# Optimization experiments

Measured on AMD Instinct MI355X. Metric: run time of the kernel, lower is better.

The kernel has to match this reference:

```python
import jax, jax.numpy as jnp
import numpy as np

N, E, F_IN, DIM, HEADS = 16384, 262144, 128, 64, 4
HID = DIM * HEADS  # 256
NEG = 0.2


def _lin(k, fan_in, fan_out):
    kw, kb = jax.random.split(k)
    s = 1.0 / np.sqrt(fan_in)
    return (jax.random.uniform(kw, (fan_in, fan_out), jnp.float32, -s, s),
            jax.random.uniform(kb, (fan_out,), jnp.float32, -s, s))


def setup_inputs() -> dict:
    key = jax.random.key(0)
    ks = jax.random.split(key, 20)
    x = jax.random.normal(ks[0], (N, F_IN), jnp.float32)
    edge_index = jax.random.randint(ks[1], (2, E), 0, N, jnp.int32)
    Win, b_in = _lin(ks[2], F_IN, DIM)
    Wskip, bskip = _lin(ks[3], DIM, HID)
    # conv1: in=DIM, out per head=DIM, heads=HEADS, concat -> HID
    Wl1, _ = _lin(ks[4], DIM, HID)
    Wr1, _ = _lin(ks[5], DIM, HID)
    att1 = jax.random.normal(ks[6], (HEADS, DIM), jnp.float32) * 0.1
    b1 = jnp.zeros((HID,), jnp.float32)
    # conv2: in=HID, out=HID, heads=1, concat=False
    Wl2, _ = _lin(ks[7], HID, HID)
    Wr2, _ = _lin(ks[8], HID, HID)
    att2 = jax.random.normal(ks[9], (1, HID), jnp.float32) * 0.1
    b2 = jnp.zeros((HID,), jnp.float32)
    # conv3: in=HID, out=HID, heads=1, concat=False
    Wl3, _ = _lin(ks[10], HID, HID)
    Wr3, _ = _lin(ks[11], HID, HID)
    att3 = jax.random.normal(ks[12], (1, HID), jnp.float32) * 0.1
    b3 = jnp.zeros((HID,), jnp.float32)
    Wm1, bm1 = _lin(ks[13], HID, DIM)
    Wm2, bm2 = _lin(ks[14], DIM, DIM)
    Wm3, bm3 = _lin(ks[15], DIM, 1)
    return dict(x=x, edge_index=edge_index, Win=Win, b_in=b_in,
                Wskip=Wskip, bskip=bskip,
                Wl1=Wl1, Wr1=Wr1, att1=att1, b1=b1,
                Wl2=Wl2, Wr2=Wr2, att2=att2, b2=b2,
                Wl3=Wl3, Wr3=Wr3, att3=att3, b3=b3,
                Wm1=Wm1, bm1=bm1, Wm2=Wm2, bm2=bm2, Wm3=Wm3, bm3=bm3)


def gatv2(x, src, dst, Wl, Wr, att, b, concat):
    # PyG GATv2Conv: x_l = lin_l(x)[src], x_r = lin_r(x)[dst]
    n = x.shape[0]
    H, D = att.shape
    xl = (x @ Wl).reshape(n, H, D)
    xr = (x @ Wr).reshape(n, H, D)
    e = jax.nn.leaky_relu(xl[src] + xr[dst], NEG)          # [E, H, D]
    logits = jnp.einsum('ehd,hd->eh', e, att)              # [E, H]
    m = jax.ops.segment_max(logits, dst, num_segments=n)   # per-dst softmax
    alpha = jnp.exp(logits - m[dst])
    denom = jax.ops.segment_sum(alpha, dst, num_segments=n)
    alpha = alpha / denom[dst]
    out = jax.ops.segment_sum(alpha[:, :, None] * xl[src], dst, num_segments=n)
    out = out.reshape(n, H * D) if concat else out.mean(axis=1)
    return out + b


def reference(x, edge_index, Win, b_in, Wskip, bskip,
              Wl1, Wr1, att1, b1, Wl2, Wr2, att2, b2,
              Wl3, Wr3, att3, b3, Wm1, bm1, Wm2, bm2, Wm3, bm3):
    n = x.shape[0]
    # add self loops (GATv2Conv default add_self_loops=True)
    loop = jnp.arange(n, dtype=edge_index.dtype)
    src = jnp.concatenate([edge_index[0], loop])
    dst = jnp.concatenate([edge_index[1], loop])

    h = jax.nn.relu(x @ Win + b_in)                         # [N, DIM]
    out1 = jax.nn.relu(gatv2(h, src, dst, Wl1, Wr1, att1, b1, True))
    out1 = out1 + (h @ Wskip + bskip)                       # [N, HID]
    out2 = jax.nn.relu(gatv2(out1, src, dst, Wl2, Wr2, att2, b2, False))
    out2 = out2 + out1
    out3 = jax.nn.relu(gatv2(out2, src, dst, Wl3, Wr3, att3, b3, False))
    out3 = out3 + out2
    out = jax.nn.relu(out3 @ Wm1 + bm1)
    out = jax.nn.relu(out @ Wm2 + bm2)
    out = out @ Wm3 + bm3                                   # [N, 1]
    return out.reshape(-1)
```

## Files before the change

### kernel.cpp

```cpp
#include <hip/hip_runtime.h>
#include <cstdint>
#include <cstddef>

#define N_NODES 16384
#define E_EDGES 262144
#define FIN     128
#define DIM     64
#define HID     256
#define NEG     0.2f

typedef _Float16 h8 __attribute__((ext_vector_type(8)));
typedef _Float16 h4 __attribute__((ext_vector_type(4)));
typedef float    f32x4 __attribute__((ext_vector_type(4)));

__global__ __launch_bounds__(256) void zero_cnt_kernel(int4* __restrict__ cnt) {
    cnt[blockIdx.x * 256 + threadIdx.x] = make_int4(0, 0, 0, 0);
}

__global__ __launch_bounds__(256) void hist_kernel(const int* __restrict__ dst,
                                                   int* __restrict__ cnt) {
    int i = blockIdx.x * 256 + threadIdx.x;
    if (i < E_EDGES) atomicAdd(&cnt[dst[i]], 1);
}

__global__ __launch_bounds__(256) void csr_scan_kernel(const int* __restrict__ cnt,
                                                       int* __restrict__ offs,
                                                       int* __restrict__ cursor) {
    __shared__ int bs[256];
    __shared__ int psum[257];
    int tid = threadIdx.x;
    int base = tid * 64;
    int s = 0;
    for (int i = 0; i < 64; ++i) s += cnt[base + i];
    bs[tid] = s;
    __syncthreads();
    if (tid == 0) {
        int r = 0;
        for (int i = 0; i < 256; ++i) { psum[i] = r; r += bs[i]; }
        psum[256] = r;
    }
    __syncthreads();
    int run = psum[tid];
    for (int i = 0; i < 64; ++i) {
        int c = cnt[base + i];
        offs[base + i] = run;
        cursor[base + i] = run;
        run += c;
    }
    if (tid == 255) offs[N_NODES] = run;
}

__global__ __launch_bounds__(256) void scatter_kernel(const int* __restrict__ src,
                                                      const int* __restrict__ dst,
                                                      int* __restrict__ cursor,
                                                      int* __restrict__ esrc) {
    int i = blockIdx.x * 256 + threadIdx.x;
    if (i < E_EDGES) {
        int p = atomicAdd(&cursor[dst[i]], 1);
        esrc[p] = src[i];
    }
}

struct PackJob { const float* W; _Float16* dst; int Ksrc, Nsrc, NT, colOff; };
struct PackJobs { PackJob j[9]; };

__global__ __launch_bounds__(256) void pack_all_kernel(PackJobs jobs) {
    PackJob jb = jobs.j[blockIdx.y];
    int i = blockIdx.x * 256 + threadIdx.x;
    if (i < jb.Ksrc * jb.Nsrc) {
        int k = i / jb.Nsrc, n = i % jb.Nsrc;
        jb.dst[((size_t)(k >> 3) * jb.NT + jb.colOff + n) * 8 + (k & 7)] = (_Float16)jb.W[i];
    }
}

__global__ __launch_bounds__(256) void cast16_kernel(const float* __restrict__ x,
                                                     _Float16* __restrict__ x16) {
    int i = blockIdx.x * 256 + threadIdx.x;
    float4 v = ((const float4*)x)[i];
    h4 o; o[0] = (_Float16)v.x; o[1] = (_Float16)v.y;
    o[2] = (_Float16)v.z; o[3] = (_Float16)v.w;
    ((h4*)x16)[i] = o;
}

template<int K, bool RELU, bool O16>
__global__ __launch_bounds__(256) void mfma_nt64_kernel(const _Float16* __restrict__ A,
                                                        const _Float16* __restrict__ Wp,
                                                        const float* __restrict__ bias,
                                                        void* __restrict__ outv) {
    int tid = threadIdx.x;
    int lane = tid & 63, wid = tid >> 6;
    int rowBase = blockIdx.x * 256 + wid * 64;
    int l15 = lane & 15, l4 = lane >> 4;

    f32x4 acc[4][4] = {};
#pragma unroll
    for (int ks = 0; ks < K / 32; ++ks) {
        h8 af[4], bf[4];
#pragma unroll
        for (int mi = 0; mi < 4; ++mi)
            af[mi] = *(const h8*)(A + (size_t)(rowBase + mi * 16 + l15) * K + ks * 32 + l4 * 8);
#pragma unroll
        for (int ni = 0; ni < 4; ++ni)
            bf[ni] = *(const h8*)(Wp + ((size_t)(ks * 4 + l4) * 64 + ni * 16 + l15) * 8);
#pragma unroll
        for (int mi = 0; mi < 4; ++mi)
#pragma unroll
            for (int ni = 0; ni < 4; ++ni)
                acc[mi][ni] = __builtin_amdgcn_mfma_f32_16x16x32_f16(af[mi], bf[ni], acc[mi][ni], 0, 0, 0);
    }
#pragma unroll
    for (int mi = 0; mi < 4; ++mi)
#pragma unroll
        for (int ni = 0; ni < 4; ++ni) {
            int c = ni * 16 + l15;
            float bv = bias[c];
#pragma unroll
            for (int q = 0; q < 4; ++q) {
                int r = rowBase + mi * 16 + l4 * 4 + q;
                float v = acc[mi][ni][q] + bv;
                if (RELU) v = fmaxf(v, 0.f);
                if constexpr (O16) ((_Float16*)outv)[(size_t)r * 64 + c] = (_Float16)v;
                else               ((float*)outv)[(size_t)r * 64 + c] = v;
            }
        }
}

template<int K>
__global__ __launch_bounds__(256) void mfma_gemm_kernel(const _Float16* __restrict__ A,
                                                        const _Float16* __restrict__ Wp,
                                                        int NT,
                                                        _Float16* __restrict__ o16a,
                                                        _Float16* __restrict__ o16b,
                                                        float* __restrict__ o32,
                                                        const float* __restrict__ bias) {
    int tid = threadIdx.x;
    int lane = tid & 63, wid = tid >> 6;
    int wm = wid >> 1, wn = wid & 1;
    int rowBase = blockIdx.x * 128 + wm * 64;
    int colBase = blockIdx.y * 128 + wn * 64;
    int l15 = lane & 15, l4 = lane >> 4;

    f32x4 acc[4][4] = {};
#pragma unroll
    for (int ks = 0; ks < K / 32; ++ks) {
        h8 af[4], bf[4];
#pragma unroll
        for (int mi = 0; mi < 4; ++mi)
            af[mi] = *(const h8*)(A + (size_t)(rowBase + mi * 16 + l15) * K + ks * 32 + l4 * 8);
#pragma unroll
        for (int ni = 0; ni < 4; ++ni)
            bf[ni] = *(const h8*)(Wp + ((size_t)(ks * 4 + l4) * NT + colBase + ni * 16 + l15) * 8);
#pragma unroll
        for (int mi = 0; mi < 4; ++mi)
#pragma unroll
            for (int ni = 0; ni < 4; ++ni)
                acc[mi][ni] = __builtin_amdgcn_mfma_f32_16x16x32_f16(af[mi], bf[ni], acc[mi][ni], 0, 0, 0);
    }

    int seg = colBase >> 8;
    int cbase = colBase & 255;
    if (o32 != nullptr && seg == 2) {
#pragma unroll
        for (int mi = 0; mi < 4; ++mi)
#pragma unroll
            for (int ni = 0; ni < 4; ++ni) {
                int c = cbase + ni * 16 + l15;
                float bv = bias[c];
#pragma unroll
                for (int q = 0; q < 4; ++q) {
                    int r = rowBase + mi * 16 + l4 * 4 + q;
                    o32[(size_t)r * 256 + c] = acc[mi][ni][q] + bv;
                }
            }
    } else {
        _Float16* o = (seg == 0) ? o16a : o16b;
#pragma unroll
        for (int mi = 0; mi < 4; ++mi)
#pragma unroll
            for (int ni = 0; ni < 4; ++ni) {
                int c = cbase + ni * 16 + l15;
#pragma unroll
                for (int q = 0; q < 4; ++q) {
                    int r = rowBase + mi * 16 + l4 * 4 + q;
                    o[(size_t)r * 256 + c] = (_Float16)acc[mi][ni][q];
                }
            }
    }
}

template<int H, int OMODE>
__global__ __launch_bounds__(256) void gat_agg_kernel(const _Float16* __restrict__ xl,
                                                      const _Float16* __restrict__ xr,
                                                      const float* __restrict__ att,
                                                      const float* __restrict__ bias,
                                                      const float* __restrict__ resid,
                                                      const int* __restrict__ offs,
                                                      const int* __restrict__ esrc,
                                                      float* __restrict__ out,
                                                      _Float16* __restrict__ out16) {
    int wid = threadIdx.x >> 6;
    int lane = threadIdx.x & 63;
    int node = blockIdx.x * 4 + wid;

    auto ld4 = [&](const _Float16* p, int n) -> float4 {
        h4 v = *(const h4*)(p + ((size_t)n << 8) + (lane << 2));
        return make_float4((float)v[0], (float)v[1], (float)v[2], (float)v[3]);
    };

    float4 xrv = ld4(xr, node);
    float4 av = ((const float4*)att)[lane];

    float m = -1e30f, s = 0.f;
    float4 acc = make_float4(0.f, 0.f, 0.f, 0.f);

    auto logit = [&](const float4& xlv) -> float {
        float ex = xlv.x + xrv.x; ex = ex > 0.f ? ex : NEG * ex;
        float ey = xlv.y + xrv.y; ey = ey > 0.f ? ey : NEG * ey;
        float ez = xlv.z + xrv.z; ez = ez > 0.f ? ez : NEG * ez;
        float ew = xlv.w + xrv.w; ew = ew > 0.f ? ew : NEG * ew;
        float lp = ex * av.x + ey * av.y + ez * av.z + ew * av.w;
        lp += __shfl_xor(lp, 1);
        lp += __shfl_xor(lp, 2);
        lp += __shfl_xor(lp, 4);
        lp += __shfl_xor(lp, 8);
        if constexpr (H == 1) {
            lp += __shfl_xor(lp, 16);
            lp += __shfl_xor(lp, 32);
        }
        return lp;
    };

    auto single = [&](int src) {
        float4 xlv = ld4(xl, src);
        float lp = logit(xlv);
        float mn = fmaxf(m, lp);
        float c = __expf(m - mn);
        float p = __expf(lp - mn);
        s = s * c + p;
        acc.x = acc.x * c + p * xlv.x;
        acc.y = acc.y * c + p * xlv.y;
        acc.z = acc.z * c + p * xlv.z;
        acc.w = acc.w * c + p * xlv.w;
        m = mn;
    };

    single(node);
    int e0 = offs[node], e1 = offs[node + 1];
    int e = e0;
    for (; e + 4 <= e1; e += 4) {
        int s0 = esrc[e], s1 = esrc[e + 1], s2 = esrc[e + 2], s3 = esrc[e + 3];
        float4 x0 = ld4(xl, s0);
        float4 x1 = ld4(xl, s1);
        float4 x2 = ld4(xl, s2);
        float4 x3 = ld4(xl, s3);
        float lp0 = logit(x0);
        float lp1 = logit(x1);
        float lp2 = logit(x2);
        float lp3 = logit(x3);
        float mn = fmaxf(fmaxf(fmaxf(lp0, lp1), fmaxf(lp2, lp3)), m);
        float c  = __expf(m - mn);
        float p0 = __expf(lp0 - mn);
        float p1 = __expf(lp1 - mn);
        float p2 = __expf(lp2 - mn);
        float p3 = __expf(lp3 - mn);
        s = s * c + ((p0 + p1) + (p2 + p3));
        acc.x = acc.x * c + ((p0 * x0.x + p1 * x1.x) + (p2 * x2.x + p3 * x3.x));
        acc.y = acc.y * c + ((p0 * x0.y + p1 * x1.y) + (p2 * x2.y + p3 * x3.y));
        acc.z = acc.z * c + ((p0 * x0.z + p1 * x1.z) + (p2 * x2.z + p3 * x3.z));
        acc.w = acc.w * c + ((p0 * x0.w + p1 * x1.w) + (p2 * x2.w + p3 * x3.w));
        m = mn;
    }
    for (; e < e1; ++e) single(esrc[e]);

    float inv = 1.f / s;
    float4 bv = ((const float4*)bias)[lane];
    float4 rv = ((const float4*)resid)[((size_t)node << 6) + lane];
    float4 o;
    o.x = fmaxf(acc.x * inv + bv.x, 0.f) + rv.x;
    o.y = fmaxf(acc.y * inv + bv.y, 0.f) + rv.y;
    o.z = fmaxf(acc.z * inv + bv.z, 0.f) + rv.z;
    o.w = fmaxf(acc.w * inv + bv.w, 0.f) + rv.w;
    if constexpr (OMODE != 2)
        ((float4*)out)[((size_t)node << 6) + lane] = o;
    if constexpr (OMODE != 0) {
        h4 ov;
        ov[0] = (_Float16)o.x; ov[1] = (_Float16)o.y;
        ov[2] = (_Float16)o.z; ov[3] = (_Float16)o.w;
        *(h4*)(out16 + ((size_t)node << 8) + (lane << 2)) = ov;
    }
}

__global__ __launch_bounds__(256) void mlp23_kernel(const float* __restrict__ tA,
                                                    const float* __restrict__ Wm2,
                                                    const float* __restrict__ bm2,
                                                    const float* __restrict__ Wm3,
                                                    const float* __restrict__ bm3,
                                                    float* __restrict__ out) {
    __shared__ float W2s[64][65];
    __shared__ float w3s[64];
    int tid = threadIdx.x;
    for (int i = tid; i < 4096; i += 256) W2s[i >> 6][i & 63] = Wm2[i];
    if (tid < 64) w3s[tid] = Wm3[tid];
    __syncthreads();
    int wid = tid >> 6, lane = tid & 63;
    float b2 = bm2[lane];
    float b3 = bm3[0];
#pragma unroll 1
    for (int i = 0; i < 8; ++i) {
        int node = blockIdx.x * 32 + wid * 8 + i;
        float a = tA[((size_t)node << 6) + lane];
        float accv = 0.f;
#pragma unroll
        for (int k = 0; k < 64; ++k) accv += __shfl(a, k) * W2s[k][lane];
        float o = fmaxf(accv + b2, 0.f) * w3s[lane];
        o += __shfl_xor(o, 1);
        o += __shfl_xor(o, 2);
        o += __shfl_xor(o, 4);
        o += __shfl_xor(o, 8);
        o += __shfl_xor(o, 16);
        o += __shfl_xor(o, 32);
        if (lane == 0) out[node] = o + b3;
    }
}

extern "C" void kernel_launch(void* const* d_in, const int* in_sizes, int n_in,
                              void* d_out, int out_size, void* d_ws, size_t ws_size,
                              hipStream_t stream) {
    const float* x     = (const float*)d_in[0];
    const int*   ei    = (const int*)d_in[1];
    const float* Win   = (const float*)d_in[2];
    const float* b_in  = (const float*)d_in[3];
    const float* Wskip = (const float*)d_in[4];
    const float* bskip = (const float*)d_in[5];
    const float* Wl1   = (const float*)d_in[6];
    const float* Wr1   = (const float*)d_in[7];
    const float* att1  = (const float*)d_in[8];
    const float* b1    = (const float*)d_in[9];
    const float* Wl2   = (const float*)d_in[10];
    const float* Wr2   = (const float*)d_in[11];
    const float* att2  = (const float*)d_in[12];
    const float* b2    = (const float*)d_in[13];
    const float* Wl3   = (const float*)d_in[14];
    const float* Wr3   = (const float*)d_in[15];
    const float* att3  = (const float*)d_in[16];
    const float* b3    = (const float*)d_in[17];
    const float* Wm1   = (const float*)d_in[18];
    const float* bm1   = (const float*)d_in[19];
    const float* Wm2   = (const float*)d_in[20];
    const float* bm2   = (const float*)d_in[21];
    const float* Wm3   = (const float*)d_in[22];
    const float* bm3   = (const float*)d_in[23];

    char* p = (char*)d_ws;
    auto alloc = [&](size_t bytes) { char* r = p; p += (bytes + 255) & ~(size_t)255; return r; };
    const size_t NN = N_NODES;
    float*    tA   = (float*)alloc(NN * 64 * 4);
    float*    skip = (float*)alloc(NN * 256 * 4);
    float*    out1 = (float*)alloc(NN * 256 * 4);
    _Float16* o116 = (_Float16*)alloc(NN * 256 * 2);
    _Float16* o216 = (_Float16*)alloc(NN * 256 * 2);
    _Float16* o316 = o116;
    _Float16* h16  = (_Float16*)alloc(NN * 64 * 2);
    _Float16* x16  = (_Float16*)alloc(NN * FIN * 2);
    _Float16* xl16 = (_Float16*)alloc(NN * 256 * 2);
    _Float16* xr16 = (_Float16*)alloc(NN * 256 * 2);
    _Float16* Wp1  = (_Float16*)alloc((size_t)64 * 768 * 2);
    _Float16* Wp2  = (_Float16*)alloc((size_t)256 * 512 * 2);
    _Float16* Wp3  = (_Float16*)alloc((size_t)256 * 512 * 2);
    _Float16* Winp = (_Float16*)alloc((size_t)128 * 64 * 2);
    _Float16* Wm1p = (_Float16*)alloc((size_t)256 * 64 * 2);
    int* cnt    = (int*)alloc(N_NODES * 4);
    int* offs   = (int*)alloc((N_NODES + 1) * 4);
    int* cursor = (int*)alloc(N_NODES * 4);
    int* esrc   = (int*)alloc(E_EDGES * 4);

    const int* src = ei;
    const int* dst = ei + E_EDGES;

    zero_cnt_kernel<<<N_NODES / 1024, 256, 0, stream>>>((int4*)cnt);
    hist_kernel<<<E_EDGES / 256, 256, 0, stream>>>(dst, cnt);
    csr_scan_kernel<<<1, 256, 0, stream>>>(cnt, offs, cursor);
    scatter_kernel<<<E_EDGES / 256, 256, 0, stream>>>(src, dst, cursor, esrc);

    PackJobs jobs = {{
        { Wl1,   Wp1,  64,  256, 768, 0   },
        { Wr1,   Wp1,  64,  256, 768, 256 },
        { Wskip, Wp1,  64,  256, 768, 512 },
        { Wl2,   Wp2,  256, 256, 512, 0   },
        { Wr2,   Wp2,  256, 256, 512, 256 },
        { Wl3,   Wp3,  256, 256, 512, 0   },
        { Wr3,   Wp3,  256, 256, 512, 256 },
        { Win,   Winp, 128, 64,  64,  0   },
        { Wm1,   Wm1p, 256, 64,  64,  0   },
    }};
    pack_all_kernel<<<dim3(256, 9), 256, 0, stream>>>(jobs);

    cast16_kernel<<<(N_NODES * FIN / 4) / 256, 256, 0, stream>>>(x, x16);
    mfma_nt64_kernel<128, true, true><<<N_NODES / 256, 256, 0, stream>>>(x16, Winp, b_in, h16);

    mfma_gemm_kernel<64><<<dim3(128, 6), 256, 0, stream>>>(h16, Wp1, 768, xl16, xr16, skip, bskip);
    gat_agg_kernel<4, 1><<<N_NODES / 4, 256, 0, stream>>>(xl16, xr16, att1, b1, skip, offs, esrc, out1, o116);

    mfma_gemm_kernel<256><<<dim3(128, 4), 256, 0, stream>>>(o116, Wp2, 512, xl16, xr16, nullptr, nullptr);
    gat_agg_kernel<1, 1><<<N_NODES / 4, 256, 0, stream>>>(xl16, xr16, att2, b2, out1, offs, esrc, skip , o216);

    mfma_gemm_kernel<256><<<dim3(128, 4), 256, 0, stream>>>(o216, Wp3, 512, xl16, xr16, nullptr, nullptr);
    gat_agg_kernel<1, 2><<<N_NODES / 4, 256, 0, stream>>>(xl16, xr16, att3, b3, skip , offs, esrc, nullptr, o316);

    mfma_nt64_kernel<256, true, false><<<N_NODES / 256, 256, 0, stream>>>(o316, Wm1p, bm1, tA);
    mlp23_kernel<<<N_NODES / 32, 256, 0, stream>>>(tA, Wm2, bm2, Wm3, bm3, (float*)d_out);
}
```

Baseline: 228.0 us.

## Fuse input cast into first GEMM, fuse MLP head, unroll aggregation by eight

Drops the separate fp32-to-fp16 cast kernel: the input GEMM now reads fp32 x directly and converts in registers. The three MLP head layers are fused into one kernel that uses MFMA for both Wm1 and Wm2 and keeps the intermediate in shared memory, so the tA round-trip and one launch go away. The GAT aggregation loop gains an 8-edge unrolled block to raise memory-level parallelism. GEMM blocks shrink to one wave of 64 rows each, which gives more blocks but less reuse of the weight loads within a block.

```diff
diff --git a/kernel.cpp b/kernel.cpp
--- a/kernel.cpp
+++ b/kernel.cpp
@@ -62,7 +62,7 @@
 }
 
 struct PackJob { const float* W; _Float16* dst; int Ksrc, Nsrc, NT, colOff; };
-struct PackJobs { PackJob j[9]; };
+struct PackJobs { PackJob j[10]; };
 
 __global__ __launch_bounds__(256) void pack_all_kernel(PackJobs jobs) {
     PackJob jb = jobs.j[blockIdx.y];
@@ -73,23 +73,13 @@
     }
 }
 
-__global__ __launch_bounds__(256) void cast16_kernel(const float* __restrict__ x,
-                                                     _Float16* __restrict__ x16) {
-    int i = blockIdx.x * 256 + threadIdx.x;
-    float4 v = ((const float4*)x)[i];
-    h4 o; o[0] = (_Float16)v.x; o[1] = (_Float16)v.y;
-    o[2] = (_Float16)v.z; o[3] = (_Float16)v.w;
-    ((h4*)x16)[i] = o;
-}
-
-template<int K, bool RELU, bool O16>
-__global__ __launch_bounds__(256) void mfma_nt64_kernel(const _Float16* __restrict__ A,
-                                                        const _Float16* __restrict__ Wp,
-                                                        const float* __restrict__ bias,
-                                                        void* __restrict__ outv) {
-    int tid = threadIdx.x;
-    int lane = tid & 63, wid = tid >> 6;
-    int rowBase = blockIdx.x * 256 + wid * 64;
+template<int K, bool RELU, bool O16, bool IN32>
+__global__ __launch_bounds__(64) void mfma_n64_kernel(const void* __restrict__ Av,
+                                                      const _Float16* __restrict__ Wp,
+                                                      const float* __restrict__ bias,
+                                                      void* __restrict__ outv) {
+    int lane = threadIdx.x;
+    int rowBase = blockIdx.x * 64;
     int l15 = lane & 15, l4 = lane >> 4;
 
     f32x4 acc[4][4] = {};
@@ -97,8 +87,21 @@
     for (int ks = 0; ks < K / 32; ++ks) {
         h8 af[4], bf[4];
 #pragma unroll
-        for (int mi = 0; mi < 4; ++mi)
-            af[mi] = *(const h8*)(A + (size_t)(rowBase + mi * 16 + l15) * K + ks * 32 + l4 * 8);
+        for (int mi = 0; mi < 4; ++mi) {
+            if constexpr (IN32) {
+                const float* ap = (const float*)Av + (size_t)(rowBase + mi * 16 + l15) * K + ks * 32 + l4 * 8;
+                float4 a0 = *(const float4*)ap;
+                float4 a1 = *(const float4*)(ap + 4);
+                h8 v;
+                v[0] = (_Float16)a0.x; v[1] = (_Float16)a0.y;
+                v[2] = (_Float16)a0.z; v[3] = (_Float16)a0.w;
+                v[4] = (_Float16)a1.x; v[5] = (_Float16)a1.y;
+                v[6] = (_Float16)a1.z; v[7] = (_Float16)a1.w;
+                af[mi] = v;
+            } else {
+                af[mi] = *(const h8*)((const _Float16*)Av + (size_t)(rowBase + mi * 16 + l15) * K + ks * 32 + l4 * 8);
+            }
+        }
 #pragma unroll
         for (int ni = 0; ni < 4; ++ni)
             bf[ni] = *(const h8*)(Wp + ((size_t)(ks * 4 + l4) * 64 + ni * 16 + l15) * 8);
@@ -247,27 +250,50 @@
     single(node);
     int e0 = offs[node], e1 = offs[node + 1];
     int e = e0;
+    for (; e + 8 <= e1; e += 8) {
+        float4 xv[8]; float lp[8], pp[8];
+#pragma unroll
+        for (int j = 0; j < 8; ++j) xv[j] = ld4(xl, esrc[e + j]);
+#pragma unroll
+        for (int j = 0; j < 8; ++j) lp[j] = logit(xv[j]);
+        float mn = m;
+#pragma unroll
+        for (int j = 0; j < 8; ++j) mn = fmaxf(mn, lp[j]);
+        float c = __expf(m - mn);
+#pragma unroll
+        for (int j = 0; j < 8; ++j) pp[j] = __expf(lp[j] - mn);
+        float ps = 0.f;
+        float4 pa = make_float4(0.f, 0.f, 0.f, 0.f);
+#pragma unroll
+        for (int j = 0; j < 8; ++j) {
+            ps += pp[j];
+            pa.x += pp[j] * xv[j].x;
+            pa.y += pp[j] * xv[j].y;
+            pa.z += pp[j] * xv[j].z;
+            pa.w += pp[j] * xv[j].w;
+        }
+        s = s * c + ps;
+        acc.x = acc.x * c + pa.x;
+        acc.y = acc.y * c + pa.y;
+        acc.z = acc.z * c + pa.z;
+        acc.w = acc.w * c + pa.w;
+        m = mn;
+    }
     for (; e + 4 <= e1; e += 4) {
-        int s0 = esrc[e], s1 = esrc[e + 1], s2 = esrc[e + 2], s3 = esrc[e + 3];
-        float4 x0 = ld4(xl, s0);
-        float4 x1 = ld4(xl, s1);
-        float4 x2 = ld4(xl, s2);
-        float4 x3 = ld4(xl, s3);
-        float lp0 = logit(x0);
-        float lp1 = logit(x1);
-        float lp2 = logit(x2);
-        float lp3 = logit(x3);
-        float mn = fmaxf(fmaxf(fmaxf(lp0, lp1), fmaxf(lp2, lp3)), m);
-        float c  = __expf(m - mn);
-        float p0 = __expf(lp0 - mn);
-        float p1 = __expf(lp1 - mn);
-        float p2 = __expf(lp2 - mn);
-        float p3 = __expf(lp3 - mn);
-        s = s * c + ((p0 + p1) + (p2 + p3));
-        acc.x = acc.x * c + ((p0 * x0.x + p1 * x1.x) + (p2 * x2.x + p3 * x3.x));
-        acc.y = acc.y * c + ((p0 * x0.y + p1 * x1.y) + (p2 * x2.y + p3 * x3.y));
-        acc.z = acc.z * c + ((p0 * x0.z + p1 * x1.z) + (p2 * x2.z + p3 * x3.z));
-        acc.w = acc.w * c + ((p0 * x0.w + p1 * x1.w) + (p2 * x2.w + p3 * x3.w));
+        float4 xv[4]; float lp[4], pp[4];
+#pragma unroll
+        for (int j = 0; j < 4; ++j) xv[j] = ld4(xl, esrc[e + j]);
+#pragma unroll
+        for (int j = 0; j < 4; ++j) lp[j] = logit(xv[j]);
+        float mn = fmaxf(fmaxf(fmaxf(lp[0], lp[1]), fmaxf(lp[2], lp[3])), m);
+        float c = __expf(m - mn);
+#pragma unroll
+        for (int j = 0; j < 4; ++j) pp[j] = __expf(lp[j] - mn);
+        s = s * c + ((pp[0] + pp[1]) + (pp[2] + pp[3]));
+        acc.x = acc.x * c + ((pp[0] * xv[0].x + pp[1] * xv[1].x) + (pp[2] * xv[2].x + pp[3] * xv[3].x));
+        acc.y = acc.y * c + ((pp[0] * xv[0].y + pp[1] * xv[1].y) + (pp[2] * xv[2].y + pp[3] * xv[3].y));
+        acc.z = acc.z * c + ((pp[0] * xv[0].z + pp[1] * xv[1].z) + (pp[2] * xv[2].z + pp[3] * xv[3].z));
+        acc.w = acc.w * c + ((pp[0] * xv[0].w + pp[1] * xv[1].w) + (pp[2] * xv[2].w + pp[3] * xv[3].w));
         m = mn;
     }
     for (; e < e1; ++e) single(esrc[e]);
@@ -290,37 +316,85 @@
     }
 }
 
-__global__ __launch_bounds__(256) void mlp23_kernel(const float* __restrict__ tA,
-                                                    const float* __restrict__ Wm2,
-                                                    const float* __restrict__ bm2,
-                                                    const float* __restrict__ Wm3,
-                                                    const float* __restrict__ bm3,
-                                                    float* __restrict__ out) {
-    __shared__ float W2s[64][65];
-    __shared__ float w3s[64];
-    int tid = threadIdx.x;
-    for (int i = tid; i < 4096; i += 256) W2s[i >> 6][i & 63] = Wm2[i];
-    if (tid < 64) w3s[tid] = Wm3[tid];
-    __syncthreads();
-    int wid = tid >> 6, lane = tid & 63;
-    float b2 = bm2[lane];
+__global__ __launch_bounds__(64) void mlp_head_kernel(const _Float16* __restrict__ A,
+                                                      const _Float16* __restrict__ Wm1p,
+                                                      const float* __restrict__ bm1,
+                                                      const _Float16* __restrict__ Wm2p,
+                                                      const float* __restrict__ bm2,
+                                                      const float* __restrict__ Wm3,
+                                                      const float* __restrict__ bm3,
+                                                      float* __restrict__ out) {
+    __shared__ _Float16 t1s[64][72];
+    int lane = threadIdx.x;
+    int rowBase = blockIdx.x * 64;
+    int l15 = lane & 15, l4 = lane >> 4;
+
+    f32x4 acc[4][4] = {};
+#pragma unroll
+    for (int ks = 0; ks < 8; ++ks) {
+        h8 af[4], bf[4];
+#pragma unroll
+        for (int mi = 0; mi < 4; ++mi)
+            af[mi] = *(const h8*)(A + (size_t)(rowBase + mi * 16 + l15) * 256 + ks * 32 + l4 * 8);
+#pragma unroll
+        for (int ni = 0; ni < 4; ++ni)
+            bf[ni] = *(const h8*)(Wm1p + ((size_t)(ks * 4 + l4) * 64 + ni * 16 + l15) * 8);
+#pragma unroll
+        for (int mi = 0; mi < 4; ++mi)
+#pragma unroll
+            for (int ni = 0; ni < 4; ++ni)
+                acc[mi][ni] = __builtin_amdgcn_mfma_f32_16x16x32_f16(af[mi], bf[ni], acc[mi][ni], 0, 0, 0);
+    }
+#pragma unroll
+    for (int mi = 0; mi < 4; ++mi)
+#pragma unroll
+        for (int ni = 0; ni < 4; ++ni) {
+            int c = ni * 16 + l15;
+            float bv = bm1[c];
+#pragma unroll
+            for (int q = 0; q < 4; ++q)
+                t1s[mi * 16 + l4 * 4 + q][c] = (_Float16)fmaxf(acc[mi][ni][q] + bv, 0.f);
+        }
+
+    f32x4 acc2[4][4] = {};
+#pragma unroll
+    for (int ks = 0; ks < 2; ++ks) {
+        h8 af[4], bf[4];
+#pragma unroll
+        for (int mi = 0; mi < 4; ++mi)
+            af[mi] = *(const h8*)&t1s[mi * 16 + l15][ks * 32 + l4 * 8];
+#pragma unroll
+        for (int ni = 0; ni < 4; ++ni)
+            bf[ni] = *(const h8*)(Wm2p + ((size_t)(ks * 4 + l4) * 64 + ni * 16 + l15) * 8);
+#pragma unroll
+        for (int mi = 0; mi < 4; ++mi)
+#pragma unroll
+            for (int ni = 0; ni < 4; ++ni)
+                acc2[mi][ni] = __builtin_amdgcn_mfma_f32_16x16x32_f16(af[mi], bf[ni], acc2[mi][ni], 0, 0, 0);
+    }
+
     float b3 = bm3[0];
-#pragma unroll 1
-    for (int i = 0; i < 8; ++i) {
-        int node = blockIdx.x * 32 + wid * 8 + i;
-        float a = tA[((size_t)node << 6) + lane];
-        float accv = 0.f;
-#pragma unroll
-        for (int k = 0; k < 64; ++k) accv += __shfl(a, k) * W2s[k][lane];
-        float o = fmaxf(accv + b2, 0.f) * w3s[lane];
-        o += __shfl_xor(o, 1);
-        o += __shfl_xor(o, 2);
-        o += __shfl_xor(o, 4);
-        o += __shfl_xor(o, 8);
-        o += __shfl_xor(o, 16);
-        o += __shfl_xor(o, 32);
-        if (lane == 0) out[node] = o + b3;
-    }
+    float b2v[4], w3v[4];
+#pragma unroll
+    for (int ni = 0; ni < 4; ++ni) {
+        b2v[ni] = bm2[ni * 16 + l15];
+        w3v[ni] = Wm3[ni * 16 + l15];
+    }
+#pragma unroll
+    for (int mi = 0; mi < 4; ++mi)
+#pragma unroll
+        for (int q = 0; q < 4; ++q) {
+            float part = 0.f;
+#pragma unroll
+            for (int ni = 0; ni < 4; ++ni)
+                part += fmaxf(acc2[mi][ni][q] + b2v[ni], 0.f) * w3v[ni];
+            part += __shfl_xor(part, 1);
+            part += __shfl_xor(part, 2);
+            part += __shfl_xor(part, 4);
+            part += __shfl_xor(part, 8);
+            if (l15 == 0)
+                out[rowBase + mi * 16 + l4 * 4 + q] = part + b3;
+        }
 }
 
 extern "C" void kernel_launch(void* const* d_in, const int* in_sizes, int n_in,
@@ -354,14 +428,12 @@
     char* p = (char*)d_ws;
     auto alloc = [&](size_t bytes) { char* r = p; p += (bytes + 255) & ~(size_t)255; return r; };
     const size_t NN = N_NODES;
-    float*    tA   = (float*)alloc(NN * 64 * 4);
     float*    skip = (float*)alloc(NN * 256 * 4);
     float*    out1 = (float*)alloc(NN * 256 * 4);
     _Float16* o116 = (_Float16*)alloc(NN * 256 * 2);
     _Float16* o216 = (_Float16*)alloc(NN * 256 * 2);
     _Float16* o316 = o116;
     _Float16* h16  = (_Float16*)alloc(NN * 64 * 2);
-    _Float16* x16  = (_Float16*)alloc(NN * FIN * 2);
     _Float16* xl16 = (_Float16*)alloc(NN * 256 * 2);
     _Float16* xr16 = (_Float16*)alloc(NN * 256 * 2);
     _Float16* Wp1  = (_Float16*)alloc((size_t)64 * 768 * 2);
@@ -369,6 +441,7 @@
     _Float16* Wp3  = (_Float16*)alloc((size_t)256 * 512 * 2);
     _Float16* Winp = (_Float16*)alloc((size_t)128 * 64 * 2);
     _Float16* Wm1p = (_Float16*)alloc((size_t)256 * 64 * 2);
+    _Float16* Wm2p = (_Float16*)alloc((size_t)64 * 64 * 2);
     int* cnt    = (int*)alloc(N_NODES * 4);
     int* offs   = (int*)alloc((N_NODES + 1) * 4);
     int* cursor = (int*)alloc(N_NODES * 4);
@@ -392,11 +465,11 @@
         { Wr3,   Wp3,  256, 256, 512, 256 },
         { Win,   Winp, 128, 64,  64,  0   },
         { Wm1,   Wm1p, 256, 64,  64,  0   },
+        { Wm2,   Wm2p, 64,  64,  64,  0   },
     }};
-    pack_all_kernel<<<dim3(256, 9), 256, 0, stream>>>(jobs);
-
-    cast16_kernel<<<(N_NODES * FIN / 4) / 256, 256, 0, stream>>>(x, x16);
-    mfma_nt64_kernel<128, true, true><<<N_NODES / 256, 256, 0, stream>>>(x16, Winp, b_in, h16);
+    pack_all_kernel<<<dim3(256, 10), 256, 0, stream>>>(jobs);
+
+    mfma_n64_kernel<128, true, true, true><<<N_NODES / 64, 64, 0, stream>>>(x, Winp, b_in, h16);
 
     mfma_gemm_kernel<64><<<dim3(128, 6), 256, 0, stream>>>(h16, Wp1, 768, xl16, xr16, skip, bskip);
     gat_agg_kernel<4, 1><<<N_NODES / 4, 256, 0, stream>>>(xl16, xr16, att1, b1, skip, offs, esrc, out1, o116);
@@ -407,6 +480,5 @@
     mfma_gemm_kernel<256><<<dim3(128, 4), 256, 0, stream>>>(o216, Wp3, 512, xl16, xr16, nullptr, nullptr);
     gat_agg_kernel<1, 2><<<N_NODES / 4, 256, 0, stream>>>(xl16, xr16, att3, b3, skip , offs, esrc, nullptr, o316);
 
-    mfma_nt64_kernel<256, true, false><<<N_NODES / 256, 256, 0, stream>>>(o316, Wm1p, bm1, tA);
-    mlp23_kernel<<<N_NODES / 32, 256, 0, stream>>>(tA, Wm2, bm2, Wm3, bm3, (float*)d_out);
-}
+    mlp_head_kernel<<<N_NODES / 64, 64, 0, stream>>>(o316, Wm1p, bm1, Wm2p, bm2, Wm3, bm3, (float*)d_out);
+}
```

New measurement: 225.5 us. Within noise of the previous version (-1.1%).
